# Kernel tuning notes

Measured on AMD Instinct MI355X. Metric: run time of the kernel, lower is better.

## Reference

```python
import jax, jax.numpy as jnp
import numpy as np

IMG = 800
FEAT_SIZES = [(200, 200), (100, 100), (50, 50), (25, 25)]
STRIDES = [4, 8, 16, 32]
ANCHOR_SIZES = [32, 64, 128, 256]
ASPECTS = np.array([0.5, 1.0, 2.0])
NA = 3
C = 128
PRE_NMS = 2000
POST_NMS = 2000
RPN_NMS_TH = 0.7
BOX_SCORE_TH = 0.05
BOX_NMS_TH = 0.5
DETS = 100
BBOX_CLIP = float(np.log(1000.0 / 16.0))
LVL_H = np.array([h for h, w in FEAT_SIZES], np.int32)
LVL_W = np.array([w for h, w in FEAT_SIZES], np.int32)
LVL_OFF = np.concatenate([[0], np.cumsum(LVL_H * LVL_W)])[:4].astype(np.int32)


def make_anchors():
    out = []
    for (h, w), stride, size in zip(FEAT_SIZES, STRIDES, ANCHOR_SIZES):
        hr = np.sqrt(ASPECTS)
        wr = 1.0 / hr
        ws = wr * size
        hs = hr * size
        base = np.round(np.stack([-ws, -hs, ws, hs], axis=1) / 2.0)  # [NA,4]
        sy = np.arange(h) * stride
        sx = np.arange(w) * stride
        yy, xx = np.meshgrid(sy, sx, indexing='ij')
        shifts = np.stack([xx.ravel(), yy.ravel(), xx.ravel(), yy.ravel()], axis=1)
        out.append((shifts[:, None, :] + base[None, :, :]).reshape(-1, 4))
    return jnp.asarray(np.concatenate(out, 0), jnp.float32)


def decode(deltas, boxes, weights):
    wx, wy, ww, wh = weights
    w = boxes[..., 2] - boxes[..., 0]
    h = boxes[..., 3] - boxes[..., 1]
    cx = boxes[..., 0] + 0.5 * w
    cy = boxes[..., 1] + 0.5 * h
    dx = deltas[..., 0] / wx
    dy = deltas[..., 1] / wy
    dw = jnp.minimum(deltas[..., 2] / ww, BBOX_CLIP)
    dh = jnp.minimum(deltas[..., 3] / wh, BBOX_CLIP)
    pcx = dx * w + cx
    pcy = dy * h + cy
    pw = jnp.exp(dw) * w
    ph = jnp.exp(dh) * h
    return jnp.stack([pcx - 0.5 * pw, pcy - 0.5 * ph, pcx + 0.5 * pw, pcy + 0.5 * ph], axis=-1)


def clip_boxes(b):
    return jnp.stack([jnp.clip(b[..., 0], 0.0, IMG), jnp.clip(b[..., 1], 0.0, IMG),
                      jnp.clip(b[..., 2], 0.0, IMG), jnp.clip(b[..., 3], 0.0, IMG)], axis=-1)


def iou_one_to_many(box, boxes):
    ix1 = jnp.maximum(box[0], boxes[:, 0])
    iy1 = jnp.maximum(box[1], boxes[:, 1])
    ix2 = jnp.minimum(box[2], boxes[:, 2])
    iy2 = jnp.minimum(box[3], boxes[:, 3])
    inter = jnp.maximum(ix2 - ix1, 0.0) * jnp.maximum(iy2 - iy1, 0.0)
    a1 = (box[2] - box[0]) * (box[3] - box[1])
    a2 = (boxes[:, 2] - boxes[:, 0]) * (boxes[:, 3] - boxes[:, 1])
    union = a1 + a2 - inter
    return jnp.where(union > 0, inter / union, 0.0)


def greedy_nms(boxes, scores, th, k):
    def step(sc, _):
        i = jnp.argmax(sc)
        s = sc[i]
        iou = iou_one_to_many(boxes[i], boxes)
        sc = jnp.where(iou > th, -jnp.inf, sc)
        sc = sc.at[i].set(-jnp.inf)
        return sc, (i, s)
    _, (idx, ss) = jax.lax.scan(step, scores, None, length=k)
    return idx, jnp.isfinite(ss)


def conv(x, w, b, pad):
    y = jax.lax.conv_general_dilated(x, w, (1, 1), [(pad, pad), (pad, pad)],
                                     dimension_numbers=('NCHW', 'OIHW', 'NCHW'))
    return y + b[None, :, None, None]


def level_map(rois):
    area = (rois[:, 2] - rois[:, 0]) * (rois[:, 3] - rois[:, 1])
    tgt = jnp.floor(4.0 + jnp.log2(jnp.sqrt(jnp.maximum(area, 0.0)) / 224.0 + 1e-6))
    return (jnp.clip(tgt, 2.0, 5.0) - 2.0).astype(jnp.int32)


def ms_roi_align(flat, rois):
    # flat: [C, total_pixels] concatenation of pyramid levels; rois: [K,4]
    K = rois.shape[0]
    lvl = level_map(rois)
    scale = jnp.asarray(1.0 / np.array(STRIDES), jnp.float32)[lvl]
    Hl = jnp.asarray(LVL_H)[lvl]
    Wl = jnp.asarray(LVL_W)[lvl]
    base = jnp.asarray(LVL_OFF)[lvl]
    x1 = rois[:, 0] * scale
    y1 = rois[:, 1] * scale
    rw = jnp.maximum(rois[:, 2] * scale - x1, 1.0)
    rh = jnp.maximum(rois[:, 3] * scale - y1, 1.0)
    off = jnp.arange(7)[:, None] + (jnp.arange(2) + 0.5)[None, :] / 2.0  # [7,2]
    ys = y1[:, None, None] + off[None] * (rh / 7.0)[:, None, None]  # [K,7,2]
    xs = x1[:, None, None] + off[None] * (rw / 7.0)[:, None, None]
    Y = jnp.broadcast_to(ys[:, :, :, None, None], (K, 7, 2, 7, 2))
    X = jnp.broadcast_to(xs[:, None, None, :, :], (K, 7, 2, 7, 2))
    Hf = Hl.astype(jnp.float32)[:, None, None, None, None]
    Wf = Wl.astype(jnp.float32)[:, None, None, None, None]
    valid = (Y > -1.0) & (Y < Hf) & (X > -1.0) & (X < Wf)
    y = jnp.clip(Y, 0.0, Hf - 1.0)
    x = jnp.clip(X, 0.0, Wf - 1.0)
    y0 = jnp.floor(y).astype(jnp.int32)
    x0 = jnp.floor(x).astype(jnp.int32)
    y1i = jnp.minimum(y0 + 1, (Hl - 1)[:, None, None, None, None])
    x1i = jnp.minimum(x0 + 1, (Wl - 1)[:, None, None, None, None])
    ly = y - y0
    lx = x - x0
    hy = 1.0 - ly
    hx = 1.0 - lx
    Wi = Wl[:, None, None, None, None]
    bi = base[:, None, None, None, None]
    def g(yi, xi):
        return flat[:, (bi + yi * Wi + xi).ravel()]  # [C, K*196]
    v = ((hy * hx).ravel() * g(y0, x0) + (hy * lx).ravel() * g(y0, x1i)
         + (ly * hx).ravel() * g(y1i, x0) + (ly * lx).ravel() * g(y1i, x1i))
    v = jnp.where(valid.ravel()[None, :], v, 0.0)
    v = v.reshape(C, K, 7, 2, 7, 2).mean(axis=(3, 5))  # avg over 2x2 samples
    return v.transpose(1, 0, 2, 3)  # [K,C,7,7]


def forward(feat0, feat1, feat2, feat3, rpn_conv_w, rpn_conv_b, rpn_cls_w, rpn_cls_b,
            rpn_bbox_w, rpn_bbox_b, fc6_w, fc6_b, fc7_w, fc7_b, cls_w, cls_b, bbox_w, bbox_b):
    feats = [feat0, feat1, feat2, feat3]
    anchors = make_anchors()
    level_sizes = [h * w * NA for (h, w) in FEAT_SIZES]
    starts = np.concatenate([[0], np.cumsum(level_sizes)])
    obj_l, del_l = [], []
    for fm in feats:
        t = jax.nn.relu(conv(fm, rpn_conv_w, rpn_conv_b, 1))
        o = conv(t, rpn_cls_w, rpn_cls_b, 0)          # [B,NA,H,W]
        d = conv(t, rpn_bbox_w, rpn_bbox_b, 0)        # [B,4*NA,H,W]
        B, _, H, W = o.shape
        obj_l.append(o.transpose(0, 2, 3, 1).reshape(B, -1))
        del_l.append(d.reshape(B, NA, 4, H, W).transpose(0, 3, 4, 1, 2).reshape(B, -1, 4))
    # torchvision RPN detaches objectness / deltas before proposal generation
    objectness = jax.lax.stop_gradient(jnp.concatenate(obj_l, 1))
    deltas = jax.lax.stop_gradient(jnp.concatenate(del_l, 1))
    proposals = decode(deltas, anchors[None, :, :], (1.0, 1.0, 1.0, 1.0))

    def rpn_filter(obj, props):
        bs, ss, ls = [], [], []
        for li in range(4):
            s, e = int(starts[li]), int(starts[li + 1])
            k = min(PRE_NMS, level_sizes[li])
            vals, idx = jax.lax.top_k(obj[s:e], k)
            bs.append(props[s:e][idx])
            ss.append(vals)
            ls.append(jnp.full((k,), li, jnp.float32))
        boxes = clip_boxes(jnp.concatenate(bs, 0))
        scores = jax.nn.sigmoid(jnp.concatenate(ss, 0))
        lvl = jnp.concatenate(ls, 0)
        ok = (boxes[:, 2] - boxes[:, 0] >= 1e-3) & (boxes[:, 3] - boxes[:, 1] >= 1e-3)
        sm = jnp.where(ok, scores, -jnp.inf)
        idx, keep = greedy_nms(boxes + (lvl * (IMG + 1.0))[:, None], sm, RPN_NMS_TH, POST_NMS)
        return boxes[idx], keep

    prop_boxes, prop_valid = jax.vmap(rpn_filter)(objectness, proposals)

    def head(rois, valid, f0, f1, f2, f3):
        flat = jnp.concatenate([f.reshape(C, -1) for f in (f0, f1, f2, f3)], axis=1)
        pooled = ms_roi_align(flat, rois)               # [K,C,7,7]
        x = pooled.reshape(POST_NMS, -1)
        x = jax.nn.relu(x @ fc6_w.T + fc6_b)
        x = jax.nn.relu(x @ fc7_w.T + fc7_b)
        logits = x @ cls_w.T + cls_b                    # [K,2]
        bdel = (x @ bbox_w.T + bbox_b).reshape(-1, 2, 4)
        boxes_all = clip_boxes(decode(bdel, rois[:, None, :], (10.0, 10.0, 5.0, 5.0)))
        scores_all = jax.nn.softmax(logits, axis=-1)
        bfg = boxes_all[:, 1]
        sfg = scores_all[:, 1]
        keep = valid & (sfg > BOX_SCORE_TH) & (bfg[:, 2] - bfg[:, 0] >= 1e-2) & (bfg[:, 3] - bfg[:, 1] >= 1e-2)
        sm = jnp.where(keep, sfg, -jnp.inf)
        idx, ok = greedy_nms(bfg, sm, BOX_NMS_TH, DETS)
        ob = jnp.where(ok[:, None], bfg[idx], 0.0)
        osc = jnp.where(ok, sfg[idx], 0.0)
        ol = jnp.where(ok, 1, 0).astype(jnp.int32)
        return ob, osc, ol

    return jax.vmap(head)(prop_boxes, prop_valid, feat0, feat1, feat2, feat3)


def setup_inputs():
    key = jax.random.key(0)
    ks = jax.random.split(key, 12)
    def rn(k, shape, s=1.0):
        return jax.random.normal(k, shape, jnp.float32) * s
    return {
        'feat0': rn(ks[0], (2, C, 200, 200)),
        'feat1': rn(ks[1], (2, C, 100, 100)),
        'feat2': rn(ks[2], (2, C, 50, 50)),
        'feat3': rn(ks[3], (2, C, 25, 25)),
        'rpn_conv_w': rn(ks[4], (C, C, 3, 3), 0.02),
        'rpn_conv_b': jnp.zeros((C,), jnp.float32),
        'rpn_cls_w': rn(ks[5], (NA, C, 1, 1), 0.02),
        'rpn_cls_b': jnp.zeros((NA,), jnp.float32),
        'rpn_bbox_w': rn(ks[6], (4 * NA, C, 1, 1), 0.02),
        'rpn_bbox_b': jnp.zeros((4 * NA,), jnp.float32),
        'fc6_w': rn(ks[7], (1024, C * 49), 0.01),
        'fc6_b': jnp.zeros((1024,), jnp.float32),
        'fc7_w': rn(ks[8], (1024, 1024), 0.01),
        'fc7_b': jnp.zeros((1024,), jnp.float32),
        'cls_w': rn(ks[9], (2, 1024), 0.01),
        'cls_b': jnp.zeros((2,), jnp.float32),
        'bbox_w': rn(ks[10], (8, 1024), 0.001),
        'bbox_b': jnp.zeros((8,), jnp.float32),
    }


def reference(feat0, feat1, feat2, feat3, rpn_conv_w, rpn_conv_b, rpn_cls_w, rpn_cls_b,
              rpn_bbox_w, rpn_bbox_b, fc6_w, fc6_b, fc7_w, fc7_b, cls_w, cls_b, bbox_w, bbox_b):
    return forward(feat0, feat1, feat2, feat3, rpn_conv_w, rpn_conv_b, rpn_cls_w, rpn_cls_b,
                   rpn_bbox_w, rpn_bbox_b, fc6_w, fc6_b, fc7_w, fc7_b, cls_w, cls_b, bbox_w, bbox_b)
```

## Files before the change

### kernel.cpp

```cpp
#include <hip/hip_runtime.h>
#include <cmath>

static constexpr int kAImg = 159375;
static constexpr int kNCand = 7875;
static constexpr int kPostNms = 2000;
static constexpr int kMPad = 2048;
static constexpr float kISC = 1.0f / 4096.0f;

__constant__ int c_AOFF[4]   = {0, 120000, 150000, 157500};
__constant__ int c_ALVL[4]   = {120000, 30000, 7500, 1875};
__constant__ int c_CBASE[4]  = {0, 2000, 4000, 6000};
__constant__ int c_LW[4]     = {200, 100, 50, 25};
__constant__ int c_LH[4]     = {200, 100, 50, 25};
__constant__ int c_STRIDE[4] = {4, 8, 16, 32};
__constant__ int c_JCHUNK[9] = {0, 118, 148, 156, 158, 276, 306, 314, 316};

struct Cand     { float x1, y1, x2, y2; unsigned key; unsigned lvl; unsigned pad0, pad1; };
struct HeadCand { float x1, y1, x2, y2; float score; unsigned key; unsigned pad0, pad1; };
struct RoiParam { int lvl; float x1, y1, rw, rh; int pad0, pad1, pad2; };
struct AnchTab  { float v[4][3][4]; };

typedef unsigned short u16;
typedef __attribute__((ext_vector_type(8))) short short8;
typedef __attribute__((ext_vector_type(4))) float f32x4;
typedef _Float16 f16x8 __attribute__((ext_vector_type(8)));

__device__ __forceinline__ unsigned keyOf(float f) {
  unsigned u = __float_as_uint(f);
  return (u & 0x80000000u) ? ~u : (u | 0x80000000u);
}

__device__ __forceinline__ void split_f16(float f, u16& hi, u16& lo) {
  union { _Float16 h; u16 u; } a, b;
  a.h = (_Float16)f;
  float r = (f - (float)a.h) * 4096.0f;
  b.h = (_Float16)r;
  hi = a.u; lo = b.u;
}

__device__ __forceinline__ unsigned long long shfl64(unsigned long long v, int src) {
  int lo = __shfl((int)(unsigned)(v & 0xffffffffull), src);
  int hi = __shfl((int)(unsigned)(v >> 32), src);
  return ((unsigned long long)(unsigned)hi << 32) | (unsigned)lo;
}

__device__ __forceinline__ float iou_pair(float4 a, float4 b) {
#pragma clang fp contract(off)
  float ix1 = fmaxf(a.x, b.x), iy1 = fmaxf(a.y, b.y);
  float ix2 = fminf(a.z, b.z), iy2 = fminf(a.w, b.w);
  float iw = fmaxf(ix2 - ix1, 0.f), ih = fmaxf(iy2 - iy1, 0.f);
  float inter = iw * ih;
  float a1 = (a.z - a.x) * (a.w - a.y);
  float a2 = (b.z - b.x) * (b.w - b.y);
  float uni = a1 + a2 - inter;
  return uni > 0.f ? inter / uni : 0.f;
}

__device__ __forceinline__ float4 decode_clip(float bx1, float by1, float bx2, float by2,
                                              float d0, float d1, float d2, float d3,
                                              float wx, float wy, float ww, float wh) {
#pragma clang fp contract(off)
  float w = bx2 - bx1, h = by2 - by1;
  float cx = bx1 + 0.5f * w, cy = by1 + 0.5f * h;
  float dx = d0 / wx, dy = d1 / wy;
  float dw = fminf(d2 / ww, 4.135166556742356f);
  float dh = fminf(d3 / wh, 4.135166556742356f);
  float pcx = dx * w + cx, pcy = dy * h + cy;
  float pw = expf(dw) * w, ph = expf(dh) * h;
  float x1 = pcx - 0.5f * pw, y1 = pcy - 0.5f * ph;
  float x2 = pcx + 0.5f * pw, y2 = pcy + 0.5f * ph;
  x1 = fminf(fmaxf(x1, 0.f), 800.f); y1 = fminf(fmaxf(y1, 0.f), 800.f);
  x2 = fminf(fmaxf(x2, 0.f), 800.f); y2 = fminf(fmaxf(y2, 0.f), 800.f);
  return make_float4(x1, y1, x2, y2);
}

__device__ __forceinline__ unsigned block_scan_bool(bool p, unsigned* wbuf, unsigned& total) {
  unsigned long long m = __ballot(p);
  int lane = threadIdx.x & 63;
  int wid = threadIdx.x >> 6;
  unsigned exc = (unsigned)__popcll(m & ((lane == 0) ? 0ull : ((~0ull) >> (64 - lane))));
  if (lane == 0) wbuf[wid] = (unsigned)__popcll(m);
  __syncthreads();
  unsigned pre = 0, tot = 0;
#pragma unroll
  for (int w = 0; w < 16; w++) { unsigned c = wbuf[w]; if (w < wid) pre += c; tot += c; }
  total = tot;
  __syncthreads();
  return pre + exc;
}

__global__ __launch_bounds__(256) void zero_u32_kernel(unsigned* __restrict__ p, int n32) {
  for (int i = blockIdx.x * 256 + threadIdx.x; i < n32; i += gridDim.x * 256) p[i] = 0u;
}

template <int H, int W>
__global__ __launch_bounds__(256) void transpose_pad_kernel(
    const float* __restrict__ feat, u16* __restrict__ Fh, u16* __restrict__ Fl) {
  __shared__ float tile[128][65];
  int y = blockIdx.y;
  int x0 = blockIdx.x * 64;
  for (int e = threadIdx.x; e < 128 * 64; e += 256) {
    int ci = e >> 6, x = e & 63;
    float v = 0.f;
    if (x0 + x < W) v = feat[(size_t)ci * (H * W) + y * W + x0 + x];
    tile[ci][x] = v;
  }
  __syncthreads();
  for (int e = threadIdx.x; e < 64 * 128; e += 256) {
    int x = e >> 7, ci = e & 127;
    if (x0 + x >= W) continue;
    u16 hi, lo;
    split_f16(tile[ci][x], hi, lo);
    size_t out = ((size_t)(y + 1) * (W + 2) + (x0 + x + 1)) * 128 + ci;
    Fh[out] = hi; Fl[out] = lo;
  }
}

__global__ __launch_bounds__(256) void conv_w_repack_kernel(
    const float* __restrict__ w3, u16* __restrict__ Wh, u16* __restrict__ Wl) {
  int idx = blockIdx.x * 256 + threadIdx.x;
  if (idx >= 9 * 128 * 128) return;
  int tap = idx >> 14;
  int r = idx & 16383;
  int co = r >> 7, ci = r & 127;
  u16 hi, lo;
  split_f16(w3[co * 1152 + ci * 9 + tap], hi, lo);
  Wh[idx] = hi; Wl[idx] = lo;
}

template <int H, int W>
__global__ __launch_bounds__(256) void conv_mfma_kernel(
    const u16* __restrict__ Fh, const u16* __restrict__ Fl,
    const u16* __restrict__ Wh, const u16* __restrict__ Wl,
    const float* __restrict__ b3, float* __restrict__ tbuf) {
  __shared__ u16 sAh[128][40], sAl[128][40], sBh[128][40], sBl[128][40];
  int tid = threadIdx.x;
  int m0 = blockIdx.x * 128;
  int w = tid >> 6, lane = tid & 63;
  int wm = (w >> 1) * 64, wn = (w & 1) * 64;
  int quad = lane >> 4, lrow = lane & 15;
  f32x4 acc1[4][4], acc2[4][4];
#pragma unroll
  for (int i = 0; i < 4; i++)
#pragma unroll
    for (int j = 0; j < 4; j++) { acc1[i][j] = (f32x4)0.f; acc2[i][j] = (f32x4)0.f; }

  for (int tap = 0; tap < 9; tap++) {
    int ky = tap / 3, kx = tap - (tap / 3) * 3;
    for (int c = 0; c < 4; c++) {
      for (int e = tid; e < 512; e += 256) {
        int row = e >> 2, seg = (e & 3) * 8;
        int m = m0 + row;
        int y = m / W, x = m - y * W;
        size_t pidx = ((size_t)(y + ky) * (W + 2) + x + kx) * 128 + c * 32 + seg;
        *(short8*)&sAh[row][seg] = *(const short8*)&Fh[pidx];
        *(short8*)&sAl[row][seg] = *(const short8*)&Fl[pidx];
        size_t bidx = ((size_t)tap * 128 + row) * 128 + c * 32 + seg;
        *(short8*)&sBh[row][seg] = *(const short8*)&Wh[bidx];
        *(short8*)&sBl[row][seg] = *(const short8*)&Wl[bidx];
      }
      __syncthreads();
      int kb = quad * 8;
      f16x8 afh[4], afl[4], bfh[4], bfl[4];
#pragma unroll
      for (int t = 0; t < 4; t++) {
        afh[t] = *(const f16x8*)&sAh[wm + t * 16 + lrow][kb];
        afl[t] = *(const f16x8*)&sAl[wm + t * 16 + lrow][kb];
        bfh[t] = *(const f16x8*)&sBh[wn + t * 16 + lrow][kb];
        bfl[t] = *(const f16x8*)&sBl[wn + t * 16 + lrow][kb];
      }
#pragma unroll
      for (int mt = 0; mt < 4; mt++)
#pragma unroll
        for (int nt = 0; nt < 4; nt++) {
          acc1[mt][nt] = __builtin_amdgcn_mfma_f32_16x16x32_f16(afh[mt], bfh[nt], acc1[mt][nt], 0, 0, 0);
          acc2[mt][nt] = __builtin_amdgcn_mfma_f32_16x16x32_f16(afh[mt], bfl[nt], acc2[mt][nt], 0, 0, 0);
          acc2[mt][nt] = __builtin_amdgcn_mfma_f32_16x16x32_f16(afl[mt], bfh[nt], acc2[mt][nt], 0, 0, 0);
        }
      __syncthreads();
    }
  }
#pragma unroll
  for (int nt = 0; nt < 4; nt++) {
    int col = wn + nt * 16 + lrow;
    float bias = b3[col];
#pragma unroll
    for (int mt = 0; mt < 4; mt++) {
#pragma unroll
      for (int reg = 0; reg < 4; reg++) {
        int row = m0 + wm + mt * 16 + quad * 4 + reg;
        float v = acc1[mt][nt][reg] + kISC * acc2[mt][nt][reg] + bias;
        tbuf[(size_t)row * 128 + col] = fmaxf(v, 0.f);
      }
    }
  }
}

__global__ __launch_bounds__(256) void head_1x1_kernel(
    const float* __restrict__ tbuf,
    const float* __restrict__ wc, const float* __restrict__ bcs,
    const float* __restrict__ wb, const float* __restrict__ bbx,
    unsigned* __restrict__ keys, float* __restrict__ deltas, int aoff, int HW) {
  __shared__ float wl[15][128];
  __shared__ float bl[15];
  for (int e = threadIdx.x; e < 15 * 128; e += 256) {
    int oc = e >> 7, k = e & 127;
    wl[oc][k] = (oc < 3) ? wc[oc * 128 + k] : wb[(oc - 3) * 128 + k];
  }
  if (threadIdx.x < 15)
    bl[threadIdx.x] = (threadIdx.x < 3) ? bcs[threadIdx.x] : bbx[threadIdx.x - 3];
  __syncthreads();
  int m = blockIdx.x * 256 + threadIdx.x;
  if (m >= HW) return;
  const float* trow = tbuf + (size_t)m * 128;
  float dot[15];
#pragma unroll
  for (int o = 0; o < 15; o++) dot[o] = 0.f;
  for (int k = 0; k < 128; k += 4) {
    float4 v = *(const float4*)&trow[k];
#pragma unroll
    for (int o = 0; o < 15; o++) {
      dot[o] = fmaf(wl[o][k], v.x, dot[o]);
      dot[o] = fmaf(wl[o][k + 1], v.y, dot[o]);
      dot[o] = fmaf(wl[o][k + 2], v.z, dot[o]);
      dot[o] = fmaf(wl[o][k + 3], v.w, dot[o]);
    }
  }
#pragma unroll
  for (int oc = 0; oc < 15; oc++) {
    float s = dot[oc] + bl[oc];
    if (oc < 3) {
      keys[aoff + m * 3 + oc] = keyOf(s);
    } else {
      int bc = oc - 3, a = bc >> 2, comp = bc & 3;
      deltas[(size_t)(aoff + m * 3 + a) * 4 + comp] = s;
    }
  }
}

__global__ __launch_bounds__(1024) void radix_select_kernel(
    const unsigned* __restrict__ keys, unsigned* __restrict__ tkT, unsigned* __restrict__ tkNeed) {
  int job = blockIdx.x;
  int b = job / 3, l = job - b * 3;
  const unsigned* kb = keys + (size_t)b * kAImg + c_AOFF[l];
  int n = c_ALVL[l];
  __shared__ unsigned hist[256];
  __shared__ unsigned s_sel, s_remk;
  unsigned prefix = 0, pmask = 0, remk = 2000;
  for (int shift = 24; shift >= 0; shift -= 8) {
    if (threadIdx.x < 256) hist[threadIdx.x] = 0;
    __syncthreads();
    for (int i = threadIdx.x; i < n; i += 1024) {
      unsigned key = kb[i];
      if ((key & pmask) == prefix) atomicAdd(&hist[(key >> shift) & 255u], 1u);
    }
    __syncthreads();
    if (threadIdx.x == 0) {
      unsigned cum = 0; int sel = 0;
      for (int d = 255; d >= 0; d--) {
        unsigned c = hist[d];
        if (cum + c >= remk) { sel = d; break; }
        cum += c;
      }
      s_sel = (unsigned)sel; s_remk = remk - cum;
    }
    __syncthreads();
    prefix |= (s_sel << shift);
// ... 279 lines not shown
  unsigned long long colNext = 0ull;
  auto issue = [&](int k) {
    int base = k * 64;
#pragma unroll
    for (int i = 0; i < 32; i++) {
      int r = base + 2 * i + half;
      pf[i] = (r < valid) ? mrow[(size_t)r * 32 + w] : 0ull;
    }
    colNext = (base + lane < valid) ? mcol[base + lane] : 0ull;
  };
  if (ntiles > 0) issue(0);

  for (int k = 0; k < ntiles; k++) {
    int base = k * 64;
    int nt = valid - base; if (nt > 64) nt = 64;
    unsigned long long col = colNext;
    unsigned long long Wrm = shfl64(removed, k);
    bool dead = (lane >= nt) || (((Wrm >> lane) & 1ull) != 0ull);
    bool kept = false;
    unsigned long long Kb = 0ull, Db = __ballot(dead);
    while (~(Kb | Db) != 0ull) {
      if (!kept && !dead) {
        if (col & Kb) dead = true;
        else if ((col & ~Db) == 0ull) kept = true;
      }
      Kb = __ballot(kept);
      Db = __ballot(dead);
    }
    int tk = __popcll(Kb);
    bool full = false;
    if (keptTotal + tk > KMAX) {
      int drop = keptTotal + tk - KMAX;
      unsigned long long kk = Kb;
      for (int d = 0; d < drop; d++) kk &= ~(1ull << (63 - __builtin_clzll(kk)));
      Kb = kk; tk = KMAX - keptTotal; full = true;
    }
    if (lane == 0) {
      unsigned long long km = Kb;
      int kc = keptTotal;
      while (km) { int t = __builtin_ctzll(km); km &= km - 1; kout[kc++] = (unsigned)(base + t); }
    }
    keptTotal += tk;
    if (full) break;
    unsigned long long acc = 0ull;
    unsigned long long kb = Kb >> half;
#pragma unroll
    for (int i = 0; i < 32; i++) {
      if ((kb >> (2 * i)) & 1ull) acc |= pf[i];
    }
    unsigned long long accOther = shfl64(acc, (lane + 32) & 63);
    if (lane < 32) removed |= acc | accOther;
    if (k + 1 < ntiles) issue(k + 1);
  }
  if (lane == 0) keptCnt[job] = (unsigned)keptTotal;
}

__global__ __launch_bounds__(256) void flag_scatter_kernel(
    const unsigned* __restrict__ keptLoc, const unsigned* __restrict__ lvlKeptCnt,
    const unsigned* __restrict__ lvlList, unsigned char* __restrict__ kflag) {
  int job = blockIdx.y;
  int k = blockIdx.x * 256 + threadIdx.x;
  if (k >= (int)lvlKeptCnt[job]) return;
  unsigned local = keptLoc[(size_t)job * 2048 + k];
  unsigned pos = lvlList[(size_t)job * 2048 + local];
  int b = job >> 2;
  kflag[(size_t)b * 8192 + pos] = 1;
}

__global__ __launch_bounds__(1024) void merge_kept_kernel(
    const unsigned char* __restrict__ kflag, const unsigned* __restrict__ validCnt,
    unsigned* __restrict__ keptIdx, unsigned* __restrict__ Mc) {
  int b = blockIdx.x;
  int valid = (int)validCnt[b];
  __shared__ unsigned wbuf[16];
  __shared__ unsigned s_run;
  if (threadIdx.x == 0) s_run = 0;
  __syncthreads();
  for (int c0 = 0; c0 < 8192; c0 += 1024) {
    int i = c0 + (int)threadIdx.x;
    bool k = (i < valid) && kflag[(size_t)b * 8192 + i];
    unsigned tot;
    unsigned exc = block_scan_bool(k, wbuf, tot);
    unsigned run = s_run;
    if (k) {
      unsigned slot = run + exc;
      if (slot < kPostNms) keptIdx[(size_t)b * kPostNms + slot] = (unsigned)i;
    }
    __syncthreads();
    if (threadIdx.x == 0) s_run = run + tot;
    __syncthreads();
  }
  if (threadIdx.x == 0) {
    unsigned r = s_run;
    Mc[b] = r < kPostNms ? r : kPostNms;
  }
}

__global__ __launch_bounds__(256) void rpn_roi_gather(
    const unsigned* __restrict__ keptIdx, const unsigned* __restrict__ Mc,
    const float4* __restrict__ boxRaw, float* __restrict__ rois) {
  int b = blockIdx.y;
  int k = blockIdx.x * 256 + threadIdx.x;
  if (k >= (int)Mc[b]) return;
  unsigned i = keptIdx[(size_t)b * kPostNms + k];
  float4 v = boxRaw[(size_t)b * 8192 + i];
  float* r = rois + ((size_t)b * kPostNms + k) * 4;
  r[0] = v.x; r[1] = v.y; r[2] = v.z; r[3] = v.w;
}

__global__ __launch_bounds__(128) void head_det_gather(
    const unsigned* __restrict__ keptIdx, const unsigned* __restrict__ cnt,
    const float4* __restrict__ hbox, const float* __restrict__ hsc,
    float* __restrict__ detBox, float* __restrict__ detSc) {
  int k = threadIdx.x;
  if (k >= (int)*cnt || k >= 100) return;
  unsigned i = keptIdx[k];
  float4 v = hbox[i];
  detBox[k * 4 + 0] = v.x; detBox[k * 4 + 1] = v.y;
  detBox[k * 4 + 2] = v.z; detBox[k * 4 + 3] = v.w;
  detSc[k] = hsc[i];
}

__global__ __launch_bounds__(256) void roi_params_kernel(
    const float* __restrict__ rois, const unsigned* __restrict__ Mc, RoiParam* __restrict__ par) {
  int b = blockIdx.y;
  int i = blockIdx.x * 256 + threadIdx.x;
  if (i >= (int)Mc[b]) return;
  const float* r = rois + ((size_t)b * kPostNms + i) * 4;
  float x1 = r[0], y1 = r[1], x2 = r[2], y2 = r[3];
  float area = (x2 - x1) * (y2 - y1);
  float tgt = floorf(4.0f + log2f(sqrtf(fmaxf(area, 0.f)) / 224.0f + 1e-6f));
  tgt = fminf(fmaxf(tgt, 2.f), 5.f);
  int l = (int)tgt - 2;
  const float scales[4] = {0.25f, 0.125f, 0.0625f, 0.03125f};
  float sc = scales[l];
  RoiParam p;
  p.lvl = l;
  p.x1 = x1 * sc; p.y1 = y1 * sc;
  p.rw = fmaxf(x2 * sc - p.x1, 1.0f);
  p.rh = fmaxf(y2 * sc - p.y1, 1.0f);
  p.pad0 = p.pad1 = p.pad2 = 0;
  par[(size_t)b * kPostNms + i] = p;
}

__global__ __launch_bounds__(256) void pad_pooled_kernel(
    u16* __restrict__ hi, u16* __restrict__ lo, const unsigned* __restrict__ Mc, int b) {
  int start = (int)Mc[b] * 6272;
  const int total = kMPad * 6272;
  for (int i = start + (int)(blockIdx.x * 256 + threadIdx.x); i < total; i += 512 * 256) {
    hi[i] = 0; lo[i] = 0;
  }
}

__global__ __launch_bounds__(256) void roi_align_kernel(
    const float* __restrict__ f0, const float* __restrict__ f1,
    const float* __restrict__ f2, const float* __restrict__ f3,
    const RoiParam* __restrict__ par, const unsigned* __restrict__ Mc,
    u16* __restrict__ pooledHi, u16* __restrict__ pooledLo, int b) {
  int idx = blockIdx.x * 256 + threadIdx.x;
  int roi = idx / 6272;
  if (roi >= (int)Mc[b]) return;
  int rem = idx - roi * 6272;
  int c = rem / 49, bin = rem - c * 49;
  int py = bin / 7, px = bin - py * 7;
  RoiParam p = par[roi];
  int H = c_LH[p.lvl], W = c_LW[p.lvl];
  const float* f = (p.lvl == 0 ? f0 : p.lvl == 1 ? f1 : p.lvl == 2 ? f2 : f3);
  f += ((size_t)b * 128 + c) * (size_t)(H * W);
  float Hf = (float)H, Wf = (float)W;
  float rh7 = p.rh / 7.0f, rw7 = p.rw / 7.0f;
  float sum = 0.f;
#pragma unroll
  for (int sy = 0; sy < 2; sy++) {
    float offy = (float)py + ((float)sy + 0.5f) * 0.5f;
    float Y = p.y1 + offy * rh7;
    float yc = fminf(fmaxf(Y, 0.f), Hf - 1.f);
    float y0f = floorf(yc);
    int y0 = (int)y0f;
    int y1 = min(y0 + 1, H - 1);
    float ly = yc - y0f, hy = 1.f - ly;
#pragma unroll
    for (int sx = 0; sx < 2; sx++) {
      float offx = (float)px + ((float)sx + 0.5f) * 0.5f;
      float X = p.x1 + offx * rw7;
      bool valid = (Y > -1.f) && (Y < Hf) && (X > -1.f) && (X < Wf);
      float xc = fminf(fmaxf(X, 0.f), Wf - 1.f);
      float x0f = floorf(xc);
      int x0 = (int)x0f;
      int x1i = min(x0 + 1, W - 1);
      float lx = xc - x0f, hx = 1.f - lx;
      float v = hy * hx * f[y0 * W + x0] + hy * lx * f[y0 * W + x1i] +
                ly * hx * f[y1 * W + x0] + ly * lx * f[y1 * W + x1i];
      sum += valid ? v : 0.f;
    }
  }
  float v = sum * 0.25f;
  u16 hi, lo;
  split_f16(v, hi, lo);
  pooledHi[idx] = hi;
  pooledLo[idx] = lo;
}

__global__ __launch_bounds__(256) void convert_split_kernel(
    const float* __restrict__ src, u16* __restrict__ hi, u16* __restrict__ lo, int n) {
  for (int i = blockIdx.x * 256 + threadIdx.x; i < n; i += gridDim.x * 256) {
    u16 h, l;
    split_f16(src[i], h, l);
    hi[i] = h; lo[i] = l;
  }
}

__global__ __launch_bounds__(256) void gemm_f16x3_kernel(
    const u16* __restrict__ Ah, const u16* __restrict__ Al,
    const u16* __restrict__ Bh, const u16* __restrict__ Bl,
    float* __restrict__ Cpart, int K, int kChunks) {
  __shared__ u16 sAh[128][40], sAl[128][40], sBh[128][40], sBl[128][40];
  int tid = threadIdx.x;
  int m0 = blockIdx.y * 128, n0 = blockIdx.x * 128;
  int kBase = blockIdx.z * kChunks * 32;
  int w = tid >> 6, lane = tid & 63;
  int wm = (w >> 1) * 64, wn = (w & 1) * 64;
  int quad = lane >> 4, lrow = lane & 15;
  f32x4 acc1[4][4], acc2[4][4];
#pragma unroll
  for (int i = 0; i < 4; i++)
#pragma unroll
    for (int j = 0; j < 4; j++) { acc1[i][j] = (f32x4)0.f; acc2[i][j] = (f32x4)0.f; }

  for (int c = 0; c < kChunks; c++) {
    int k0 = kBase + c * 32;
    for (int e = tid; e < 512; e += 256) {
      int row = e >> 2, kk = (e & 3) * 8;
      size_t ga = (size_t)(m0 + row) * K + k0 + kk;
      size_t gb = (size_t)(n0 + row) * K + k0 + kk;
      *(short8*)&sAh[row][kk] = *(const short8*)&Ah[ga];
      *(short8*)&sAl[row][kk] = *(const short8*)&Al[ga];
      *(short8*)&sBh[row][kk] = *(const short8*)&Bh[gb];
      *(short8*)&sBl[row][kk] = *(const short8*)&Bl[gb];
    }
    __syncthreads();
    int kb = quad * 8;
    f16x8 afh[4], afl[4], bfh[4], bfl[4];
#pragma unroll
    for (int t = 0; t < 4; t++) {
      afh[t] = *(const f16x8*)&sAh[wm + t * 16 + lrow][kb];
      afl[t] = *(const f16x8*)&sAl[wm + t * 16 + lrow][kb];
      bfh[t] = *(const f16x8*)&sBh[wn + t * 16 + lrow][kb];
      bfl[t] = *(const f16x8*)&sBl[wn + t * 16 + lrow][kb];
    }
#pragma unroll
    for (int mt = 0; mt < 4; mt++)
#pragma unroll
      for (int nt = 0; nt < 4; nt++) {
        acc1[mt][nt] = __builtin_amdgcn_mfma_f32_16x16x32_f16(afh[mt], bfh[nt], acc1[mt][nt], 0, 0, 0);
        acc2[mt][nt] = __builtin_amdgcn_mfma_f32_16x16x32_f16(afh[mt], bfl[nt], acc2[mt][nt], 0, 0, 0);
        acc2[mt][nt] = __builtin_amdgcn_mfma_f32_16x16x32_f16(afl[mt], bfh[nt], acc2[mt][nt], 0, 0, 0);
      }
    __syncthreads();
  }
  float* out = Cpart + (size_t)blockIdx.z * (kMPad * 1024);
#pragma unroll
  for (int mt = 0; mt < 4; mt++)
#pragma unroll
    for (int nt = 0; nt < 4; nt++) {
      int col = n0 + wn + nt * 16 + lrow;
#pragma unroll
      for (int reg = 0; reg < 4; reg++) {
        int row = m0 + wm + mt * 16 + quad * 4 + reg;
        out[(size_t)row * 1024 + col] = acc1[mt][nt][reg] + kISC * acc2[mt][nt][reg];
      }
    }
}

__global__ __launch_bounds__(256) void combine_relu_split_kernel(
    const float* __restrict__ part, const float* __restrict__ bias,
    u16* __restrict__ hi, u16* __restrict__ lo) {
  int idx = blockIdx.x * 256 + threadIdx.x;
  int n = idx & 1023;
  float v = fmaxf(part[idx] + part[idx + kMPad * 1024] + bias[n], 0.f);
  u16 h, l;
  split_f16(v, h, l);
  hi[idx] = h; lo[idx] = l;
}

__global__ __launch_bounds__(256) void combine_relu_f32_kernel(
    const float* __restrict__ part, const float* __restrict__ bias,
    float* __restrict__ out) {
  int idx = blockIdx.x * 256 + threadIdx.x;
  int n = idx & 1023;
  out[idx] = fmaxf(part[idx] + part[idx + kMPad * 1024] + bias[n], 0.f);
}

__global__ __launch_bounds__(64) void head_linear_kernel(
    const float* __restrict__ H2, const float* __restrict__ cw, const float* __restrict__ cb2,
    const float* __restrict__ bw, const float* __restrict__ bb2,
    const unsigned* __restrict__ Mc, float* __restrict__ out10) {
  int r = blockIdx.x;
  if (r >= (int)*Mc) return;
  __shared__ float x[1024];
  const float* h = H2 + (size_t)r * 1024;
  for (int i = threadIdx.x; i < 1024; i += 64) x[i] = h[i];
  __syncthreads();
  int t = threadIdx.x;
  if (t < 10) {
    const float* w = (t < 2) ? (cw + t * 1024) : (bw + (t - 2) * 1024);
    float bias = (t < 2) ? cb2[t] : bb2[t - 2];
    float dot = 0.f;
    for (int k = 0; k < 1024; k++) dot = fmaf(w[k], x[k], dot);
    out10[r * 10 + t] = dot + bias;
  }
}

__global__ __launch_bounds__(256) void head_decode_kernel(
    const float* __restrict__ out10, const float* __restrict__ rois,
    const unsigned* __restrict__ Mc, HeadCand* __restrict__ hc, int b) {
#pragma clang fp contract(off)
  int r = blockIdx.x * 256 + threadIdx.x;
  if (r >= (int)Mc[b]) return;
  const float* h = out10 + (size_t)r * 10;
  float l0 = h[0], l1 = h[1];
  float mx = fmaxf(l0, l1);
  float e0 = expf(l0 - mx), e1 = expf(l1 - mx);
  float sfg = e1 / (e0 + e1);
  const float* rr = rois + ((size_t)b * kPostNms + r) * 4;
  float4 bx = decode_clip(rr[0], rr[1], rr[2], rr[3], h[6], h[7], h[8], h[9],
                          10.f, 10.f, 5.f, 5.f);
  bool keep = (sfg > 0.05f) && (bx.z - bx.x >= 0.01f) && (bx.w - bx.y >= 0.01f);
  HeadCand c;
  c.x1 = bx.x; c.y1 = bx.y; c.x2 = bx.z; c.y2 = bx.w;
  c.score = sfg;
  c.key = keep ? keyOf(sfg) : 0u;
  c.pad0 = c.pad1 = 0;
  hc[r] = c;
}

__global__ __launch_bounds__(256) void output_kernel(
    const float* __restrict__ detBox, const float* __restrict__ detSc,
    const unsigned* __restrict__ detCnt, float* __restrict__ out) {
  int t = threadIdx.x;
  if (t >= 200) return;
  int b = t / 100, q = t - b * 100;
  int cnt = (int)detCnt[b];
  float bx0 = 0.f, bx1 = 0.f, bx2 = 0.f, bx3 = 0.f, sc = 0.f, lb = 0.f;
  if (q < cnt) {
    const float* d = detBox + ((size_t)b * 100 + q) * 4;
    bx0 = d[0]; bx1 = d[1]; bx2 = d[2]; bx3 = d[3];
    sc = detSc[b * 100 + q];
    lb = 1.0f;
  }
  float* ob = out + ((size_t)b * 100 + q) * 4;
  ob[0] = bx0; ob[1] = bx1; ob[2] = bx2; ob[3] = bx3;
  out[800 + t] = sc;
  out[1000 + t] = lb;
}

extern "C" void kernel_launch(void* const* d_in, const int* in_sizes, int n_in,
                              void* d_out, int out_size, void* d_ws, size_t ws_size,
                              hipStream_t stream) {
  (void)in_sizes; (void)n_in; (void)out_size; (void)ws_size;
  const float* feats[4] = {(const float*)d_in[0], (const float*)d_in[1],
                           (const float*)d_in[2], (const float*)d_in[3]};
  const float* w3 = (const float*)d_in[4];
  const float* b3 = (const float*)d_in[5];
  const float* wc = (const float*)d_in[6];
  const float* bcs = (const float*)d_in[7];
  const float* wb = (const float*)d_in[8];
  const float* bbx = (const float*)d_in[9];
  const float* fc6w = (const float*)d_in[10];
  const float* fc6b = (const float*)d_in[11];
  const float* fc7w = (const float*)d_in[12];
  const float* fc7b = (const float*)d_in[13];
  const float* clsw = (const float*)d_in[14];
  const float* clsb = (const float*)d_in[15];
  const float* bboxw = (const float*)d_in[16];
  const float* bboxb = (const float*)d_in[17];

  unsigned char* base = (unsigned char*)d_ws;
  size_t off = 0;
  auto alloc = [&](size_t bytes) -> void* {
    void* p = base + off;
    off += (bytes + 255) & ~(size_t)255;
    return p;
  };
  unsigned* keys = (unsigned*)alloc((size_t)2 * kAImg * 4);
  float* deltas = (float*)alloc((size_t)2 * kAImg * 16);
  unsigned* tkT = (unsigned*)alloc(32);
  unsigned* tkNeed = (unsigned*)alloc(32);
  unsigned* gtCnt = (unsigned*)alloc(316 * 4);
  unsigned* eqCnt = (unsigned*)alloc(316 * 4);
  unsigned* gtBase = (unsigned*)alloc(316 * 4);
  unsigned* eqBase = (unsigned*)alloc(316 * 4);
  Cand* cand = (Cand*)alloc((size_t)2 * kNCand * sizeof(Cand));
  unsigned* sortedSlot = (unsigned*)alloc((size_t)2 * 8192 * 4);
  unsigned* validCnt = (unsigned*)alloc(8);
  float4* boxRaw = (float4*)alloc((size_t)2 * 8192 * 16);
  float4* boxLvl = (float4*)alloc((size_t)8 * 2048 * 16);
  unsigned* lvlList = (unsigned*)alloc((size_t)8 * 2048 * 4);
  unsigned* lvlCnt = (unsigned*)alloc(32);
  unsigned long long* lvlMask = (unsigned long long*)alloc((size_t)8 * 2048 * 32 * 8);
  unsigned long long* lvlCol = (unsigned long long*)alloc((size_t)8 * 2048 * 8);
  unsigned* keptLoc = (unsigned*)alloc((size_t)8 * 2048 * 4);
  unsigned* lvlKeptCnt = (unsigned*)alloc(32);
  unsigned char* kflag = (unsigned char*)alloc((size_t)2 * 8192);
  unsigned* keptIdx = (unsigned*)alloc((size_t)2 * kPostNms * 4);
  float* rois = (float*)alloc((size_t)2 * kPostNms * 16);
  unsigned* Mc = (unsigned*)alloc(8);
  RoiParam* roiPar = (RoiParam*)alloc((size_t)2 * kPostNms * sizeof(RoiParam));
  u16* padHi = (u16*)alloc((size_t)204 * 202 * 128 * 2);
  u16* padLo = (u16*)alloc((size_t)204 * 202 * 128 * 2);
  u16* wTapHi = (u16*)alloc((size_t)9 * 128 * 128 * 2);
  u16* wTapLo = (u16*)alloc((size_t)9 * 128 * 128 * 2);
  float* tbuf = (float*)alloc((size_t)313 * 128 * 128 * 4);
  u16* pooledHi = (u16*)alloc((size_t)kMPad * 6272 * 2);
  u16* pooledLo = (u16*)alloc((size_t)kMPad * 6272 * 2);
  u16* fc6wHi = (u16*)alloc((size_t)1024 * 6272 * 2);
  u16* fc6wLo = (u16*)alloc((size_t)1024 * 6272 * 2);
  u16* fc7wHi = (u16*)alloc((size_t)1024 * 1024 * 2);
  u16* fc7wLo = (u16*)alloc((size_t)1024 * 1024 * 2);
  float* part = (float*)alloc((size_t)2 * kMPad * 1024 * 4);
  u16* H1hi = (u16*)alloc((size_t)kMPad * 1024 * 2);
  u16* H1lo = (u16*)alloc((size_t)kMPad * 1024 * 2);
  float* H2buf = (float*)alloc((size_t)kMPad * 1024 * 4);
  float* out10 = (float*)alloc((size_t)kPostNms * 10 * 4);
  HeadCand* hc = (HeadCand*)alloc((size_t)kPostNms * sizeof(HeadCand));
  unsigned* hsorted = (unsigned*)alloc((size_t)2048 * 4);
  unsigned* hvalid = (unsigned*)alloc(4);
  float4* hbox = (float4*)alloc((size_t)2048 * 16);
  float* hsc = (float*)alloc((size_t)2048 * 4);
  unsigned long long* hMask = (unsigned long long*)alloc((size_t)2048 * 32 * 8);
  unsigned long long* hCol = (unsigned long long*)alloc((size_t)2048 * 8);
  unsigned* hkept = (unsigned*)alloc((size_t)128 * 4);
  float* detBox = (float*)alloc((size_t)2 * 100 * 4 * 4);
  float* detSc = (float*)alloc((size_t)2 * 100 * 4);
  unsigned* detCnt = (unsigned*)alloc(8);

  AnchTab tab;
  {
    const double aspects[3] = {0.5, 1.0, 2.0};
    const int sizes[4] = {32, 64, 128, 256};
    for (int l = 0; l < 4; l++)
      for (int a = 0; a < 3; a++) {
        double hr = sqrt(aspects[a]);
        double wr = 1.0 / hr;
        double wsz = wr * sizes[l], hsz = hr * sizes[l];
        tab.v[l][a][0] = (float)rint(-wsz / 2.0);
        tab.v[l][a][1] = (float)rint(-hsz / 2.0);
        tab.v[l][a][2] = (float)rint(wsz / 2.0);
        tab.v[l][a][3] = (float)rint(hsz / 2.0);
      }
  }

  const int LH[4] = {200, 100, 50, 25}, LW[4] = {200, 100, 50, 25};
  const int AOFF[4] = {0, 120000, 150000, 157500};

  convert_split_kernel<<<4096, 256, 0, stream>>>(fc6w, fc6wHi, fc6wLo, 1024 * 6272);
  convert_split_kernel<<<1024, 256, 0, stream>>>(fc7w, fc7wHi, fc7wLo, 1024 * 1024);
  conv_w_repack_kernel<<<(9 * 128 * 128 + 255) / 256, 256, 0, stream>>>(w3, wTapHi, wTapLo);

  for (int b = 0; b < 2; b++) {
    for (int l = 0; l < 4; l++) {
      int H = LH[l], W = LW[l];
      int HW = H * W;
      int mtiles = (HW + 127) / 128;
      int n32 = (H + 4) * (W + 2) * 128 / 2;
      zero_u32_kernel<<<512, 256, 0, stream>>>((unsigned*)padHi, n32);
      zero_u32_kernel<<<512, 256, 0, stream>>>((unsigned*)padLo, n32);
      const float* fsrc = feats[l] + (size_t)b * 128 * HW;
      dim3 tgrid((W + 63) / 64, H);
      switch (l) {
        case 0:
          transpose_pad_kernel<200, 200><<<tgrid, 256, 0, stream>>>(fsrc, padHi, padLo);
          conv_mfma_kernel<200, 200><<<mtiles, 256, 0, stream>>>(padHi, padLo, wTapHi, wTapLo, b3, tbuf);
          break;
        case 1:
          transpose_pad_kernel<100, 100><<<tgrid, 256, 0, stream>>>(fsrc, padHi, padLo);
          conv_mfma_kernel<100, 100><<<mtiles, 256, 0, stream>>>(padHi, padLo, wTapHi, wTapLo, b3, tbuf);
          break;
        case 2:
          transpose_pad_kernel<50, 50><<<tgrid, 256, 0, stream>>>(fsrc, padHi, padLo);
          conv_mfma_kernel<50, 50><<<mtiles, 256, 0, stream>>>(padHi, padLo, wTapHi, wTapLo, b3, tbuf);
          break;
        default:
          transpose_pad_kernel<25, 25><<<tgrid, 256, 0, stream>>>(fsrc, padHi, padLo);
          conv_mfma_kernel<25, 25><<<mtiles, 256, 0, stream>>>(padHi, padLo, wTapHi, wTapLo, b3, tbuf);
          break;
      }
      head_1x1_kernel<<<(HW + 255) / 256, 256, 0, stream>>>(
          tbuf, wc, bcs, wb, bbx, keys + (size_t)b * kAImg,
          deltas + (size_t)b * kAImg * 4, AOFF[l], HW);
    }
  }

  radix_select_kernel<<<6, 1024, 0, stream>>>(keys, tkT, tkNeed);
  cand_count_kernel<<<316, 1024, 0, stream>>>(keys, tkT, gtCnt, eqCnt);
  cand_prefix_kernel<<<1, 512, 0, stream>>>(gtCnt, eqCnt, gtBase, eqBase);
  cand_scatter_kernel<<<316, 1024, 0, stream>>>(
      keys, deltas, tkT, tkNeed, gtBase, eqBase, cand, tab);
  sort_desc_kernel<8192><<<2, 1024, 0, stream>>>(
      ((const unsigned*)cand) + 4, 8, kNCand, nullptr, sortedSlot, validCnt, kNCand * 8, 8192);
  rpn_sort_gather<<<dim3(32, 2), 256, 0, stream>>>(cand, sortedSlot, validCnt, boxRaw);
  lvl_compact_kernel<<<2, 1024, 0, stream>>>(cand, sortedSlot, validCnt, boxLvl, lvlList, lvlCnt);
  nms_mask_kernel<<<dim3(32, 32, 8), 64, 0, stream>>>(
      boxLvl, lvlCnt, lvlMask, 32, 2048, (long long)2048 * 32, 0.7f);
  nms_col_kernel<<<dim3(32, 8), 64, 0, stream>>>(
      boxLvl, lvlCnt, lvlCol, 2048, 2048, 0.7f);
  nms_reduce_frontier_kernel<2048><<<8, 64, 0, stream>>>(
      lvlMask, lvlCol, lvlCnt, keptLoc, lvlKeptCnt, (long long)2048 * 32, 2048);
  zero_u32_kernel<<<16, 256, 0, stream>>>((unsigned*)kflag, 4096);
  flag_scatter_kernel<<<dim3(8, 8), 256, 0, stream>>>(keptLoc, lvlKeptCnt, lvlList, kflag);
  merge_kept_kernel<<<2, 1024, 0, stream>>>(kflag, validCnt, keptIdx, Mc);
  rpn_roi_gather<<<dim3(8, 2), 256, 0, stream>>>(keptIdx, Mc, boxRaw, rois);
  roi_params_kernel<<<dim3(8, 2), 256, 0, stream>>>(rois, Mc, roiPar);

  for (int b = 0; b < 2; b++) {
    pad_pooled_kernel<<<512, 256, 0, stream>>>(pooledHi, pooledLo, Mc, b);
    roi_align_kernel<<<49000, 256, 0, stream>>>(
        feats[0], feats[1], feats[2], feats[3], roiPar + (size_t)b * kPostNms, Mc,
        pooledHi, pooledLo, b);
    gemm_f16x3_kernel<<<dim3(8, 16, 2), 256, 0, stream>>>(
        pooledHi, pooledLo, fc6wHi, fc6wLo, part, 6272, 98);
    combine_relu_split_kernel<<<8192, 256, 0, stream>>>(part, fc6b, H1hi, H1lo);
    gemm_f16x3_kernel<<<dim3(8, 16, 2), 256, 0, stream>>>(
        H1hi, H1lo, fc7wHi, fc7wLo, part, 1024, 16);
    combine_relu_f32_kernel<<<8192, 256, 0, stream>>>(part, fc7b, H2buf);
    head_linear_kernel<<<2000, 64, 0, stream>>>(H2buf, clsw, clsb, bboxw, bboxb, Mc + b, out10);
    head_decode_kernel<<<8, 256, 0, stream>>>(out10, rois, Mc, hc, b);
    sort_desc_kernel<2048><<<1, 1024, 0, stream>>>(
        ((const unsigned*)hc) + 5, 8, 2000, Mc + b, hsorted, hvalid, 0, 0);
    head_sort_gather<<<8, 256, 0, stream>>>(hc, hsorted, hvalid, hbox, hsc);
    nms_mask_kernel<<<dim3(32, 32, 1), 64, 0, stream>>>(
        hbox, hvalid, hMask, 32, 0, 0, 0.5f);
    nms_col_kernel<<<dim3(32, 1), 64, 0, stream>>>(
        hbox, hvalid, hCol, 0, 0, 0.5f);
    nms_reduce_frontier_kernel<100><<<1, 64, 0, stream>>>(
        hMask, hCol, hvalid, hkept, detCnt + b, (long long)2048 * 32, 0);
    head_det_gather<<<1, 128, 0, stream>>>(
        hkept, detCnt + b, hbox, hsc, detBox + (size_t)b * 400, detSc + (size_t)b * 100);
  }
  output_kernel<<<1, 256, 0, stream>>>(detBox, detSc, detCnt, (float*)d_out);
}
```

Baseline: 2.360 ms.

## Use channel-last feature layout for RoIAlign and permute fc6 weights to match

The transpose kernel now also writes an fp32 HWC copy of each feature level. RoIAlign assigns one wave per (roi, bin), with each lane loading two adjacent channels as a float2, so bilinear gathers become coalesced and the sampling coordinates are computed once per bin instead of once per channel. The pooled layout changes to bin-major, channel-minor, so fc6 weights are permuted into the same order during conversion. This costs an extra HWC buffer write and a strided read when converting the fc6 weights.

```diff
diff --git a/kernel.cpp b/kernel.cpp
--- a/kernel.cpp
+++ b/kernel.cpp
@@ -5,6 +5,7 @@
 static constexpr int kNCand = 7875;
 static constexpr int kPostNms = 2000;
 static constexpr int kMPad = 2048;
+static constexpr int kHWCImg = 53125;
 static constexpr float kISC = 1.0f / 4096.0f;
 
 __constant__ int c_AOFF[4]   = {0, 120000, 150000, 157500};
@@ -13,6 +14,7 @@
 __constant__ int c_LW[4]     = {200, 100, 50, 25};
 __constant__ int c_LH[4]     = {200, 100, 50, 25};
 __constant__ int c_STRIDE[4] = {4, 8, 16, 32};
+__constant__ int c_POFF[4]   = {0, 40000, 50000, 52500};
 __constant__ int c_JCHUNK[9] = {0, 118, 148, 156, 158, 276, 306, 314, 316};
 
 struct Cand     { float x1, y1, x2, y2; unsigned key; unsigned lvl; unsigned pad0, pad1; };
@@ -95,7 +97,8 @@
 
 template <int H, int W>
 __global__ __launch_bounds__(256) void transpose_pad_kernel(
-    const float* __restrict__ feat, u16* __restrict__ Fh, u16* __restrict__ Fl) {
+    const float* __restrict__ feat, u16* __restrict__ Fh, u16* __restrict__ Fl,
+    float* __restrict__ Fw) {
   __shared__ float tile[128][65];
   int y = blockIdx.y;
   int x0 = blockIdx.x * 64;
@@ -109,10 +112,12 @@
   for (int e = threadIdx.x; e < 64 * 128; e += 256) {
     int x = e >> 7, ci = e & 127;
     if (x0 + x >= W) continue;
+    float v = tile[ci][x];
     u16 hi, lo;
-    split_f16(tile[ci][x], hi, lo);
+    split_f16(v, hi, lo);
     size_t out = ((size_t)(y + 1) * (W + 2) + (x0 + x + 1)) * 128 + ci;
     Fh[out] = hi; Fl[out] = lo;
+    Fw[((size_t)y * W + (x0 + x)) * 128 + ci] = v;
   }
 }
 
@@ -698,24 +703,23 @@
   }
 }
 
-__global__ __launch_bounds__(256) void roi_align_kernel(
-    const float* __restrict__ f0, const float* __restrict__ f1,
-    const float* __restrict__ f2, const float* __restrict__ f3,
-    const RoiParam* __restrict__ par, const unsigned* __restrict__ Mc,
-    u16* __restrict__ pooledHi, u16* __restrict__ pooledLo, int b) {
-  int idx = blockIdx.x * 256 + threadIdx.x;
-  int roi = idx / 6272;
+__global__ __launch_bounds__(256) void roi_align_hwc_kernel(
+    const float* __restrict__ fhwc, const RoiParam* __restrict__ par,
+    const unsigned* __restrict__ Mc, u16* __restrict__ pooledHi,
+    u16* __restrict__ pooledLo, int b) {
+  int wave = blockIdx.x * 4 + (int)(threadIdx.x >> 6);
+  int lane = threadIdx.x & 63;
+  int roi = wave / 49;
   if (roi >= (int)Mc[b]) return;
-  int rem = idx - roi * 6272;
-  int c = rem / 49, bin = rem - c * 49;
+  int bin = wave - roi * 49;
   int py = bin / 7, px = bin - py * 7;
   RoiParam p = par[roi];
   int H = c_LH[p.lvl], W = c_LW[p.lvl];
-  const float* f = (p.lvl == 0 ? f0 : p.lvl == 1 ? f1 : p.lvl == 2 ? f2 : f3);
-  f += ((size_t)b * 128 + c) * (size_t)(H * W);
+  const float* f = fhwc + ((size_t)b * kHWCImg + c_POFF[p.lvl]) * 128;
   float Hf = (float)H, Wf = (float)W;
   float rh7 = p.rh / 7.0f, rw7 = p.rw / 7.0f;
-  float sum = 0.f;
+  int c0 = lane * 2;
+  float acc0 = 0.f, acc1 = 0.f;
 #pragma unroll
   for (int sy = 0; sy < 2; sy++) {
     float offy = (float)py + ((float)sy + 0.5f) * 0.5f;
@@ -735,16 +739,27 @@
       int x0 = (int)x0f;
       int x1i = min(x0 + 1, W - 1);
       float lx = xc - x0f, hx = 1.f - lx;
-      float v = hy * hx * f[y0 * W + x0] + hy * lx * f[y0 * W + x1i] +
-                ly * hx * f[y1 * W + x0] + ly * lx * f[y1 * W + x1i];
-      sum += valid ? v : 0.f;
-    }
-  }
-  float v = sum * 0.25f;
-  u16 hi, lo;
-  split_f16(v, hi, lo);
-  pooledHi[idx] = hi;
-  pooledLo[idx] = lo;
+      if (valid) {
+        const float* p00 = f + ((size_t)y0 * W + x0) * 128 + c0;
+        const float* p01 = f + ((size_t)y0 * W + x1i) * 128 + c0;
+        const float* p10 = f + ((size_t)y1 * W + x0) * 128 + c0;
+        const float* p11 = f + ((size_t)y1 * W + x1i) * 128 + c0;
+        float2 v00 = *(const float2*)p00;
+        float2 v01 = *(const float2*)p01;
+        float2 v10 = *(const float2*)p10;
+        float2 v11 = *(const float2*)p11;
+        acc0 += hy * hx * v00.x + hy * lx * v01.x + ly * hx * v10.x + ly * lx * v11.x;
+        acc1 += hy * hx * v00.y + hy * lx * v01.y + ly * hx * v10.y + ly * lx * v11.y;
+      }
+    }
+  }
+  float va = acc0 * 0.25f, vb = acc1 * 0.25f;
+  u16 h0, l0, h1, l1;
+  split_f16(va, h0, l0);
+  split_f16(vb, h1, l1);
+  size_t o = (size_t)roi * 6272 + bin * 128 + c0;
+  *(unsigned*)&pooledHi[o] = (unsigned)h0 | ((unsigned)h1 << 16);
+  *(unsigned*)&pooledLo[o] = (unsigned)l0 | ((unsigned)l1 << 16);
 }
 
 __global__ __launch_bounds__(256) void convert_split_kernel(
@@ -754,6 +769,17 @@
     split_f16(src[i], h, l);
     hi[i] = h; lo[i] = l;
   }
+}
+
+__global__ __launch_bounds__(256) void convert_split_fc6_kernel(
+    const float* __restrict__ src, u16* __restrict__ hi, u16* __restrict__ lo) {
+  int d = blockIdx.x * 256 + threadIdx.x;
+  if (d >= 1024 * 6272) return;
+  int n = d / 6272, r = d - n * 6272;
+  int bin = r >> 7, c = r & 127;
+  u16 h, l;
+  split_f16(src[n * 6272 + c * 49 + bin], h, l);
+  hi[d] = h; lo[d] = l;
 }
 
 __global__ __launch_bounds__(256) void gemm_f16x3_kernel(
@@ -957,6 +983,7 @@
   u16* wTapHi = (u16*)alloc((size_t)9 * 128 * 128 * 2);
   u16* wTapLo = (u16*)alloc((size_t)9 * 128 * 128 * 2);
   float* tbuf = (float*)alloc((size_t)313 * 128 * 128 * 4);
+  float* fhwc = (float*)alloc((size_t)2 * kHWCImg * 128 * 4);
   u16* pooledHi = (u16*)alloc((size_t)kMPad * 6272 * 2);
   u16* pooledLo = (u16*)alloc((size_t)kMPad * 6272 * 2);
   u16* fc6wHi = (u16*)alloc((size_t)1024 * 6272 * 2);
@@ -998,8 +1025,9 @@
 
   const int LH[4] = {200, 100, 50, 25}, LW[4] = {200, 100, 50, 25};
   const int AOFF[4] = {0, 120000, 150000, 157500};
-
-  convert_split_kernel<<<4096, 256, 0, stream>>>(fc6w, fc6wHi, fc6wLo, 1024 * 6272);
+  const int POFF[4] = {0, 40000, 50000, 52500};
+
+  convert_split_fc6_kernel<<<(1024 * 6272 + 255) / 256, 256, 0, stream>>>(fc6w, fc6wHi, fc6wLo);
   convert_split_kernel<<<1024, 256, 0, stream>>>(fc7w, fc7wHi, fc7wLo, 1024 * 1024);
   conv_w_repack_kernel<<<(9 * 128 * 128 + 255) / 256, 256, 0, stream>>>(w3, wTapHi, wTapLo);
 
@@ -1012,22 +1040,23 @@
       zero_u32_kernel<<<512, 256, 0, stream>>>((unsigned*)padHi, n32);
       zero_u32_kernel<<<512, 256, 0, stream>>>((unsigned*)padLo, n32);
       const float* fsrc = feats[l] + (size_t)b * 128 * HW;
+      float* fdst = fhwc + ((size_t)b * kHWCImg + POFF[l]) * 128;
       dim3 tgrid((W + 63) / 64, H);
       switch (l) {
         case 0:
-          transpose_pad_kernel<200, 200><<<tgrid, 256, 0, stream>>>(fsrc, padHi, padLo);
+          transpose_pad_kernel<200, 200><<<tgrid, 256, 0, stream>>>(fsrc, padHi, padLo, fdst);
           conv_mfma_kernel<200, 200><<<mtiles, 256, 0, stream>>>(padHi, padLo, wTapHi, wTapLo, b3, tbuf);
           break;
         case 1:
-          transpose_pad_kernel<100, 100><<<tgrid, 256, 0, stream>>>(fsrc, padHi, padLo);
+          transpose_pad_kernel<100, 100><<<tgrid, 256, 0, stream>>>(fsrc, padHi, padLo, fdst);
           conv_mfma_kernel<100, 100><<<mtiles, 256, 0, stream>>>(padHi, padLo, wTapHi, wTapLo, b3, tbuf);
           break;
         case 2:
-          transpose_pad_kernel<50, 50><<<tgrid, 256, 0, stream>>>(fsrc, padHi, padLo);
+          transpose_pad_kernel<50, 50><<<tgrid, 256, 0, stream>>>(fsrc, padHi, padLo, fdst);
           conv_mfma_kernel<50, 50><<<mtiles, 256, 0, stream>>>(padHi, padLo, wTapHi, wTapLo, b3, tbuf);
           break;
         default:
-          transpose_pad_kernel<25, 25><<<tgrid, 256, 0, stream>>>(fsrc, padHi, padLo);
+          transpose_pad_kernel<25, 25><<<tgrid, 256, 0, stream>>>(fsrc, padHi, padLo, fdst);
           conv_mfma_kernel<25, 25><<<mtiles, 256, 0, stream>>>(padHi, padLo, wTapHi, wTapLo, b3, tbuf);
           break;
       }
@@ -1060,9 +1089,8 @@
 
   for (int b = 0; b < 2; b++) {
     pad_pooled_kernel<<<512, 256, 0, stream>>>(pooledHi, pooledLo, Mc, b);
-    roi_align_kernel<<<49000, 256, 0, stream>>>(
-        feats[0], feats[1], feats[2], feats[3], roiPar + (size_t)b * kPostNms, Mc,
-        pooledHi, pooledLo, b);
+    roi_align_hwc_kernel<<<(kPostNms * 49 + 3) / 4, 256, 0, stream>>>(
+        fhwc, roiPar + (size_t)b * kPostNms, Mc, pooledHi, pooledLo, b);
     gemm_f16x3_kernel<<<dim3(8, 16, 2), 256, 0, stream>>>(
         pooledHi, pooledLo, fc6wHi, fc6wLo, part, 6272, 98);
     combine_relu_split_kernel<<<8192, 256, 0, stream>>>(part, fc6b, H1hi, H1lo);
```

Result: faster. 2.203 ms (-6.6%).
